# Kernel optimization log

Measured on AMD Instinct MI355X. Metric: run time of the kernel, lower is better.

## Reference

```python
import jax, jax.numpy as jnp
import numpy as np

B, N, C, H, M, CC = 8, 1024, 1280, 20, 77, 768
FF = 4 * C
AQ_BITS = 8
W_BITS = 8


def fq_sym(x, bits=AQ_BITS):
    # per-tensor symmetric fake quant with straight-through estimator
    qmax = 2.0 ** (bits - 1) - 1.0
    delta = jnp.maximum(jnp.max(jnp.abs(x)), 1e-8) / qmax
    q = jnp.clip(jnp.round(x / delta), -qmax - 1.0, qmax) * delta
    return x + jax.lax.stop_gradient(q - x)


def fq_zero(x, bits=W_BITS):
    # asymmetric, always_zero (zero point = 0): for softmax probs in [0,1]
    levels = 2.0 ** bits - 1.0
    delta = jnp.maximum(jnp.max(x), 1e-8) / levels
    q = jnp.clip(jnp.round(x / delta), 0.0, levels) * delta
    return x + jax.lax.stop_gradient(q - x)


def layer_norm(x, g, b, eps=1e-5):
    mu = jnp.mean(x, axis=-1, keepdims=True)
    var = jnp.var(x, axis=-1, keepdims=True)
    return (x - mu) * jax.lax.rsqrt(var + eps) * g + b


def attention(x, ctx, Wq, Wk, Wv, Wo, bo, heads):
    b, n, c = x.shape
    m = ctx.shape[1]
    dh = c // heads
    q = fq_sym(x @ Wq)
    k = fq_sym(ctx @ Wk)
    v = fq_sym(ctx @ Wv)
    q = q.reshape(b, n, heads, dh).transpose(0, 2, 1, 3)
    k = k.reshape(b, m, heads, dh).transpose(0, 2, 1, 3)
    v = v.reshape(b, m, heads, dh).transpose(0, 2, 1, 3)
    scores = jnp.einsum('bhnd,bhmd->bhnm', q, k) * (dh ** -0.5)
    w = jax.nn.softmax(scores, axis=-1)
    w = fq_zero(w)  # quantized softmax weights (forces explicit prob materialization)
    out = jnp.einsum('bhnm,bhmd->bhnd', w, v)
    out = out.transpose(0, 2, 1, 3).reshape(b, n, c)
    return out @ Wo + bo


def geglu_ff(x, W1, b1, W2, b2):
    h = x @ W1 + b1
    a, g = jnp.split(h, 2, axis=-1)
    return (a * jax.nn.gelu(g)) @ W2 + b2


def setup_inputs() -> dict:
    key = jax.random.key(0)
    ks = jax.random.split(key, 16)
    s = 0.02
    return {
        'x': jax.random.normal(ks[0], (B, N, C), jnp.float32),
        'ctx': jax.random.normal(ks[1], (B, M, CC), jnp.float32),
        'ln1_g': jnp.ones((C,), jnp.float32), 'ln1_b': jnp.zeros((C,), jnp.float32),
        'ln2_g': jnp.ones((C,), jnp.float32), 'ln2_b': jnp.zeros((C,), jnp.float32),
        'ln3_g': jnp.ones((C,), jnp.float32), 'ln3_b': jnp.zeros((C,), jnp.float32),
        'Wq1': jax.random.normal(ks[2], (C, C), jnp.float32) * s,
        'Wk1': jax.random.normal(ks[3], (C, C), jnp.float32) * s,
        'Wv1': jax.random.normal(ks[4], (C, C), jnp.float32) * s,
        'Wo1': jax.random.normal(ks[5], (C, C), jnp.float32) * s,
        'bo1': jnp.zeros((C,), jnp.float32),
        'Wq2': jax.random.normal(ks[6], (C, C), jnp.float32) * s,
        'Wk2': jax.random.normal(ks[7], (CC, C), jnp.float32) * s,
        'Wv2': jax.random.normal(ks[8], (CC, C), jnp.float32) * s,
        'Wo2': jax.random.normal(ks[9], (C, C), jnp.float32) * s,
        'bo2': jnp.zeros((C,), jnp.float32),
        'Wff1': jax.random.normal(ks[10], (C, 2 * FF), jnp.float32) * s,
        'bff1': jnp.zeros((2 * FF,), jnp.float32),
        'Wff2': jax.random.normal(ks[11], (FF, C), jnp.float32) * s,
        'bff2': jnp.zeros((C,), jnp.float32),
        'heads': H,
    }


def reference(x, ctx, ln1_g, ln1_b, ln2_g, ln2_b, ln3_g, ln3_b,
              Wq1, Wk1, Wv1, Wo1, bo1, Wq2, Wk2, Wv2, Wo2, bo2,
              Wff1, bff1, Wff2, bff2, heads):
    h = attention(layer_norm(x, ln1_g, ln1_b), layer_norm(x, ln1_g, ln1_b),
                  Wq1, Wk1, Wv1, Wo1, bo1, heads)
    x = x + h
    h = attention(layer_norm(x, ln2_g, ln2_b), ctx, Wq2, Wk2, Wv2, Wo2, bo2, heads)
    x = x + h
    x = x + geglu_ff(layer_norm(x, ln3_g, ln3_b), Wff1, bff1, Wff2, bff2)
    return x
```

## Files before the change

### kernel.cpp

```cpp
#include <hip/hip_runtime.h>

typedef __attribute__((ext_vector_type(8))) short bf16x8;
typedef __attribute__((ext_vector_type(4))) float f32x4;

#define DEV __device__ __forceinline__
#define MF(A, B, CACC) CACC = __builtin_amdgcn_mfma_f32_16x16x32_bf16(A, B, CACC, 0, 0, 0)

DEV ushort f2b(float f) {
  unsigned u = __float_as_uint(f);
  u += 0x7fffu + ((u >> 16) & 1u);
  return (ushort)(u >> 16);
}
DEV float b2f(ushort u) { return __uint_as_float(((unsigned)u) << 16); }

DEV void gl_lds16(ushort* lds_base, const ushort* gp) {
  __builtin_amdgcn_global_load_lds(
      (__attribute__((address_space(1))) const void*)gp,
      (__attribute__((address_space(3))) void*)lds_base, 16, 0, 0);
}

__global__ void k_zero(unsigned* p, int n) {
  int i = blockIdx.x * blockDim.x + threadIdx.x;
  if (i < n) p[i] = 0u;
}
// ... 76 lines not shown
    if (rbase + 0 < M) st1(v0, rbase + 0, c_, ldc, resid, Cf, Cb);
    if (rbase + 1 < M) st1(v1, rbase + 1, c_, ldc, resid, Cf, Cb);
    if (rbase + 2 < M) st1(v2, rbase + 2, c_, ldc, resid, Cf, Cb);
    if (rbase + 3 < M) st1(v3, rbase + 3, c_, ldc, resid, Cf, Cb);
  }
  return am;
}

__global__ __launch_bounds__(256) void k_gemm(
    const ushort* __restrict__ A, int lda,
    const ushort* __restrict__ BT, int ldb,
    float* __restrict__ Cf, ushort* __restrict__ Cb, int ldc,
    const float* __restrict__ bias, const float* __restrict__ resid,
    unsigned* am_slot, int M, int N, int K, int slcN) {
  __shared__ __align__(16) ushort SAB[8192];
  int tid = threadIdx.x;
  int wave = tid >> 6, lane = tid & 63;
  int q = lane >> 4, mi = lane & 15;
  int wr = (wave >> 1) * 64, wc = (wave & 1) * 64;
  int bm0 = blockIdx.y * 128, bn0 = blockIdx.x * 128;
  f32x4 c00 = {}, c01 = {}, c02 = {}, c03 = {};
  f32x4 c10 = {}, c11 = {}, c12 = {}, c13 = {};
  f32x4 c20 = {}, c21 = {}, c22 = {}, c23 = {};
  f32x4 c30 = {}, c31 = {}, c32 = {}, c33 = {};
  for (int k0 = 0; k0 < K; k0 += 32) {
    __syncthreads();
    #pragma unroll
    for (int t = 0; t < 4; t++) {
      int c = wave * 256 + t * 64 + lane;
      const ushort* gp;
      if (c < 512) {
        int r = c >> 2, kc = (c & 3) << 3;
        int gr = bm0 + r; if (gr >= M) gr = M - 1;
        gp = A + (size_t)gr * lda + k0 + kc;
      } else {
        int c2 = c - 512;
        int r = c2 >> 2, kc = (c2 & 3) << 3;
        int gn = bn0 + r; if (gn >= N) gn = N - 1;
        gp = BT + (size_t)gn * ldb + k0 + kc;
      }
      gl_lds16(&SAB[(wave * 256 + t * 64) * 8], gp);
    }
    __syncthreads();
    const ushort* Ab = &SAB[(wr + mi) * 32 + q * 8];
    const ushort* Bb = &SAB[4096 + (wc + mi) * 32 + q * 8];
    bf16x8 a0 = *(const bf16x8*)(Ab);
    bf16x8 a1 = *(const bf16x8*)(Ab + 512);
    bf16x8 a2 = *(const bf16x8*)(Ab + 1024);
    bf16x8 a3 = *(const bf16x8*)(Ab + 1536);
    bf16x8 b0 = *(const bf16x8*)(Bb);
    bf16x8 b1 = *(const bf16x8*)(Bb + 512);
    bf16x8 b2 = *(const bf16x8*)(Bb + 1024);
    bf16x8 b3 = *(const bf16x8*)(Bb + 1536);
    MF(a0, b0, c00); MF(a0, b1, c01); MF(a0, b2, c02); MF(a0, b3, c03);
    MF(a1, b0, c10); MF(a1, b1, c11); MF(a1, b2, c12); MF(a1, b3, c13);
    MF(a2, b0, c20); MF(a2, b1, c21); MF(a2, b2, c22); MF(a2, b3, c23);
    MF(a3, b0, c30); MF(a3, b1, c31); MF(a3, b2, c32); MF(a3, b3, c33);
  }
  int rb = bm0 + wr + q * 4, cb = bn0 + wc + mi;
  float am = 0.f;
  am = fmaxf(am, epi4(c00, rb +  0, cb +  0, M, N, ldc, bias, resid, Cf, Cb));
  am = fmaxf(am, epi4(c01, rb +  0, cb + 16, M, N, ldc, bias, resid, Cf, Cb));
  am = fmaxf(am, epi4(c02, rb +  0, cb + 32, M, N, ldc, bias, resid, Cf, Cb));
  am = fmaxf(am, epi4(c03, rb +  0, cb + 48, M, N, ldc, bias, resid, Cf, Cb));
  am = fmaxf(am, epi4(c10, rb + 16, cb +  0, M, N, ldc, bias, resid, Cf, Cb));
  am = fmaxf(am, epi4(c11, rb + 16, cb + 16, M, N, ldc, bias, resid, Cf, Cb));
  am = fmaxf(am, epi4(c12, rb + 16, cb + 32, M, N, ldc, bias, resid, Cf, Cb));
  am = fmaxf(am, epi4(c13, rb + 16, cb + 48, M, N, ldc, bias, resid, Cf, Cb));
  am = fmaxf(am, epi4(c20, rb + 32, cb +  0, M, N, ldc, bias, resid, Cf, Cb));
  am = fmaxf(am, epi4(c21, rb + 32, cb + 16, M, N, ldc, bias, resid, Cf, Cb));
  am = fmaxf(am, epi4(c22, rb + 32, cb + 32, M, N, ldc, bias, resid, Cf, Cb));
  am = fmaxf(am, epi4(c23, rb + 32, cb + 48, M, N, ldc, bias, resid, Cf, Cb));
  am = fmaxf(am, epi4(c30, rb + 48, cb +  0, M, N, ldc, bias, resid, Cf, Cb));
  am = fmaxf(am, epi4(c31, rb + 48, cb + 16, M, N, ldc, bias, resid, Cf, Cb));
  am = fmaxf(am, epi4(c32, rb + 48, cb + 32, M, N, ldc, bias, resid, Cf, Cb));
  am = fmaxf(am, epi4(c33, rb + 48, cb + 48, M, N, ldc, bias, resid, Cf, Cb));
  if (am_slot) {
    #pragma unroll
    for (int off = 32; off; off >>= 1) am = fmaxf(am, __shfl_down(am, off));
    if (lane == 0) atomicMax(am_slot + bn0 / slcN, __float_as_uint(am));
  }
}

__global__ void k_quant3(const ushort* __restrict__ in, ushort* __restrict__ out,
                         const unsigned* __restrict__ slotb, int n,
                         int colw, int ld, int slcw) {
  int i = blockIdx.x * 256 + threadIdx.x;
  if (i >= n) return;
  int row = i / colw, col = i - row * colw;
  size_t a = (size_t)row * ld + col;
  float delta = fmaxf(__uint_as_float(slotb[col / slcw]), 1e-8f) * (1.f / 127.f);
  float x = b2f(in[a]);
  float y = fminf(fmaxf(rintf(x / delta), -128.f), 127.f) * delta;
  out[a] = f2b(y);
}

__global__ __launch_bounds__(256) void k_vt(const ushort* __restrict__ vq,
    ushort* __restrict__ vT, int H, int Mr, int Mpad, int ldv) {
  __shared__ __align__(16) ushort T[64][72];
  int bh = blockIdx.y, b = bh / H, h = bh % H;
  int m0 = blockIdx.x * 64;
  int tid = threadIdx.x;
  #pragma unroll
  for (int c = tid; c < 512; c += 256) {
    int mm = c >> 3, dc = (c & 7) << 3;
    int m = m0 + mm;
    int4 val = make_int4(0, 0, 0, 0);
    if (m < Mr) val = *(const int4*)(vq + ((size_t)b * Mr + m) * ldv + h * 64 + dc);
    *(int4*)&T[mm][dc] = val;
  }
  __syncthreads();
  #pragma unroll
  for (int c = tid; c < 512; c += 256) {
    int dd = c >> 3, mc = (c & 7) << 3;
    unsigned w0 = (unsigned)T[mc + 0][dd] | ((unsigned)T[mc + 1][dd] << 16);
    unsigned w1 = (unsigned)T[mc + 2][dd] | ((unsigned)T[mc + 3][dd] << 16);
    unsigned w2 = (unsigned)T[mc + 4][dd] | ((unsigned)T[mc + 5][dd] << 16);
    unsigned w3 = (unsigned)T[mc + 6][dd] | ((unsigned)T[mc + 7][dd] << 16);
    int4 val = make_int4((int)w0, (int)w1, (int)w2, (int)w3);
    *(int4*)(vT + ((size_t)bh * 64 + dd) * Mpad + m0 + mc) = val;
  }
}

__global__ __launch_bounds__(256) void k_attn1(
    const ushort* __restrict__ qq, const ushort* __restrict__ kq,
    float2* __restrict__ rs, unsigned* __restrict__ pmax,
    int H, int N, int Mr, int ldq, int ldk, float cs) {
  __shared__ __align__(16) ushort Qs[64][72];
  __shared__ __align__(16) ushort Ks[64][72];
  int tid = threadIdx.x;
  int wave = tid >> 6, lane = tid & 63;
  int q = lane >> 4, mi = lane & 15;
  int bh = blockIdx.y, b = bh / H, h = bh % H;
  int r0 = blockIdx.x * 64;
  #pragma unroll
  for (int c = tid; c < 512; c += 256) {
    int r = c >> 3, dc = (c & 7) << 3;
    *(int4*)&Qs[r][dc] = *(const int4*)(qq + ((size_t)b * N + r0 + r) * ldq + h * 64 + dc);
  }
  float m_run = -3.0e38f, z_run = 0.f;
  int nt = (Mr + 63) >> 6;
  for (int mt = 0; mt < nt; mt++) {
    __syncthreads();
    #pragma unroll
    for (int c = tid; c < 512; c += 256) {
      int mm = c >> 3, dc = (c & 7) << 3;
      int m = mt * 64 + mm;
      int4 val = make_int4(0, 0, 0, 0);
      if (m < Mr) val = *(const int4*)(kq + ((size_t)b * Mr + m) * ldk + h * 64 + dc);
      *(int4*)&Ks[mm][dc] = val;
    }
    __syncthreads();
    f32x4 s0 = {}, s1 = {}, s2 = {}, s3 = {};
    #pragma unroll
    for (int kc = 0; kc < 2; kc++) {
      bf16x8 qv  = *(const bf16x8*)&Qs[wave * 16 + mi][kc * 32 + q * 8];
      bf16x8 k0v = *(const bf16x8*)&Ks[mi][kc * 32 + q * 8];
      bf16x8 k1v = *(const bf16x8*)&Ks[16 + mi][kc * 32 + q * 8];
      bf16x8 k2v = *(const bf16x8*)&Ks[32 + mi][kc * 32 + q * 8];
      bf16x8 k3v = *(const bf16x8*)&Ks[48 + mi][kc * 32 + q * 8];
      MF(k0v, qv, s0); MF(k1v, qv, s1); MF(k2v, qv, s2); MF(k3v, qv, s3);
    }
    int kb = mt * 64 + q * 4;
    float e0  = (kb + 0  < Mr) ? s0.x * cs : -3.0e38f;
    float e1  = (kb + 1  < Mr) ? s0.y * cs : -3.0e38f;
    float e2  = (kb + 2  < Mr) ? s0.z * cs : -3.0e38f;
    float e3  = (kb + 3  < Mr) ? s0.w * cs : -3.0e38f;
    float e4  = (kb + 16 < Mr) ? s1.x * cs : -3.0e38f;
    float e5  = (kb + 17 < Mr) ? s1.y * cs : -3.0e38f;
    float e6  = (kb + 18 < Mr) ? s1.z * cs : -3.0e38f;
    float e7  = (kb + 19 < Mr) ? s1.w * cs : -3.0e38f;
    float e8  = (kb + 32 < Mr) ? s2.x * cs : -3.0e38f;
    float e9  = (kb + 33 < Mr) ? s2.y * cs : -3.0e38f;
    float e10 = (kb + 34 < Mr) ? s2.z * cs : -3.0e38f;
    float e11 = (kb + 35 < Mr) ? s2.w * cs : -3.0e38f;
    float e12 = (kb + 48 < Mr) ? s3.x * cs : -3.0e38f;
    float e13 = (kb + 49 < Mr) ? s3.y * cs : -3.0e38f;
    float e14 = (kb + 50 < Mr) ? s3.z * cs : -3.0e38f;
    float e15 = (kb + 51 < Mr) ? s3.w * cs : -3.0e38f;
    float tm = fmaxf(fmaxf(fmaxf(fmaxf(e0, e1), fmaxf(e2, e3)),
                           fmaxf(fmaxf(e4, e5), fmaxf(e6, e7))),
                     fmaxf(fmaxf(fmaxf(e8, e9), fmaxf(e10, e11)),
                           fmaxf(fmaxf(e12, e13), fmaxf(e14, e15))));
    float mn = fmaxf(m_run, tm);
    float zs = exp2f(e0 - mn)  + exp2f(e1 - mn)  + exp2f(e2 - mn)  + exp2f(e3 - mn)
             + exp2f(e4 - mn)  + exp2f(e5 - mn)  + exp2f(e6 - mn)  + exp2f(e7 - mn)
             + exp2f(e8 - mn)  + exp2f(e9 - mn)  + exp2f(e10 - mn) + exp2f(e11 - mn)
             + exp2f(e12 - mn) + exp2f(e13 - mn) + exp2f(e14 - mn) + exp2f(e15 - mn);
    z_run = z_run * exp2f(m_run - mn) + zs;
    m_run = mn;
  }
  float mo = fmaxf(m_run, __shfl_xor(m_run, 16));
  mo = fmaxf(mo, __shfl_xor(mo, 32));
  float zz = z_run * exp2f(m_run - mo);
  zz += __shfl_xor(zz, 16);
  zz += __shfl_xor(zz, 32);
  if (q == 0) {
    float2 st; st.x = mo; st.y = zz;
    rs[(size_t)bh * N + r0 + wave * 16 + mi] = st;
  }
  float pm = 1.f / zz;
  #pragma unroll
  for (int off = 32; off; off >>= 1) pm = fmaxf(pm, __shfl_down(pm, off));
  if (lane == 0) atomicMax(pmax, __float_as_uint(pm));
}

DEV ushort q8lvl(float s, float cs, float mc) {
  float p = fminf(rintf(exp2f(fmaf(s, cs, -mc))), 255.f);
  return (ushort)(__float_as_uint(p) >> 16);
}

__global__ __launch_bounds__(256) void k_attn2(
    const ushort* __restrict__ qq, const ushort* __restrict__ kq,
    const ushort* __restrict__ vT, const float2* __restrict__ rs,
    const unsigned* __restrict__ pmax, ushort* __restrict__ ao,
    int H, int N, int Mr, int Mpad, int ldq, int ldk, float cs) {
  const int C = 1280;
  __shared__ __align__(16) ushort Qs[64][72];
  __shared__ __align__(16) ushort Ks[64][72];
  __shared__ __align__(16) ushort Vs[64][72];
  __shared__ __align__(16) ushort Ps[64][72];
  int tid = threadIdx.x;
  int wave = tid >> 6, lane = tid & 63;
  int q = lane >> 4, mi = lane & 15;
  int bh = blockIdx.y, b = bh / H, h = bh % H;
  int r0 = blockIdx.x * 64;
  #pragma unroll
  for (int c = tid; c < 512; c += 256) {
    int r = c >> 3, dc = (c & 7) << 3;
    *(int4*)&Qs[r][dc] = *(const int4*)(qq + ((size_t)b * N + r0 + r) * ldq + h * 64 + dc);
  }
  int rbase = wave * 16 + q * 4;
  float delta = fmaxf(__uint_as_float(*pmax), 1e-8f) * (1.f / 255.f);
  float ld = __log2f(delta);
  float2 st0 = rs[(size_t)bh * N + r0 + rbase + 0];
  float2 st1 = rs[(size_t)bh * N + r0 + rbase + 1];
  float2 st2 = rs[(size_t)bh * N + r0 + rbase + 2];
  float2 st3 = rs[(size_t)bh * N + r0 + rbase + 3];
  float mc0 = st0.x + __log2f(st0.y) + ld;
  float mc1 = st1.x + __log2f(st1.y) + ld;
  float mc2 = st2.x + __log2f(st2.y) + ld;
  float mc3 = st3.x + __log2f(st3.y) + ld;
  f32x4 o0 = {}, o1 = {}, o2 = {}, o3 = {};
  int nt = (Mr + 63) >> 6;
  for (int mt = 0; mt < nt; mt++) {
    __syncthreads();
    #pragma unroll
    for (int c = tid; c < 512; c += 256) {
      int mm = c >> 3, dc = (c & 7) << 3;
      int m = mt * 64 + mm;
      int4 val = make_int4(0, 0, 0, 0);
      if (m < Mr) val = *(const int4*)(kq + ((size_t)b * Mr + m) * ldk + h * 64 + dc);
      *(int4*)&Ks[mm][dc] = val;
      *(int4*)&Vs[mm][dc] = *(const int4*)(vT + ((size_t)bh * 64 + mm) * Mpad + mt * 64 + dc);
    }
    __syncthreads();
    f32x4 s0 = {}, s1 = {}, s2 = {}, s3 = {};
    #pragma unroll
    for (int kc = 0; kc < 2; kc++) {
      bf16x8 aq  = *(const bf16x8*)&Qs[wave * 16 + mi][kc * 32 + q * 8];
      bf16x8 k0v = *(const bf16x8*)&Ks[mi][kc * 32 + q * 8];
      bf16x8 k1v = *(const bf16x8*)&Ks[16 + mi][kc * 32 + q * 8];
      bf16x8 k2v = *(const bf16x8*)&Ks[32 + mi][kc * 32 + q * 8];
      bf16x8 k3v = *(const bf16x8*)&Ks[48 + mi][kc * 32 + q * 8];
      MF(aq, k0v, s0); MF(aq, k1v, s1); MF(aq, k2v, s2); MF(aq, k3v, s3);
    }
    int mlim = Mr - mt * 64;
    bool ok0 = (mi      < mlim);
    bool ok1 = (16 + mi < mlim);
    bool ok2 = (32 + mi < mlim);
    bool ok3 = (48 + mi < mlim);
    Ps[rbase + 0][mi]      = ok0 ? q8lvl(s0.x, cs, mc0) : (ushort)0;
    Ps[rbase + 1][mi]      = ok0 ? q8lvl(s0.y, cs, mc1) : (ushort)0;
    Ps[rbase + 2][mi]      = ok0 ? q8lvl(s0.z, cs, mc2) : (ushort)0;
    Ps[rbase + 3][mi]      = ok0 ? q8lvl(s0.w, cs, mc3) : (ushort)0;
    Ps[rbase + 0][16 + mi] = ok1 ? q8lvl(s1.x, cs, mc0) : (ushort)0;
    Ps[rbase + 1][16 + mi] = ok1 ? q8lvl(s1.y, cs, mc1) : (ushort)0;
    Ps[rbase + 2][16 + mi] = ok1 ? q8lvl(s1.z, cs, mc2) : (ushort)0;
    Ps[rbase + 3][16 + mi] = ok1 ? q8lvl(s1.w, cs, mc3) : (ushort)0;
    Ps[rbase + 0][32 + mi] = ok2 ? q8lvl(s2.x, cs, mc0) : (ushort)0;
    Ps[rbase + 1][32 + mi] = ok2 ? q8lvl(s2.y, cs, mc1) : (ushort)0;
    Ps[rbase + 2][32 + mi] = ok2 ? q8lvl(s2.z, cs, mc2) : (ushort)0;
    Ps[rbase + 3][32 + mi] = ok2 ? q8lvl(s2.w, cs, mc3) : (ushort)0;
    Ps[rbase + 0][48 + mi] = ok3 ? q8lvl(s3.x, cs, mc0) : (ushort)0;
    Ps[rbase + 1][48 + mi] = ok3 ? q8lvl(s3.y, cs, mc1) : (ushort)0;
    Ps[rbase + 2][48 + mi] = ok3 ? q8lvl(s3.z, cs, mc2) : (ushort)0;
    Ps[rbase + 3][48 + mi] = ok3 ? q8lvl(s3.w, cs, mc3) : (ushort)0;
    asm volatile("s_waitcnt lgkmcnt(0)" ::: "memory");
    __builtin_amdgcn_sched_barrier(0);
    #pragma unroll
    for (int kc = 0; kc < 2; kc++) {
      bf16x8 ap = *(const bf16x8*)&Ps[wave * 16 + mi][kc * 32 + q * 8];
      bf16x8 v0 = *(const bf16x8*)&Vs[mi][kc * 32 + q * 8];
      bf16x8 v1 = *(const bf16x8*)&Vs[16 + mi][kc * 32 + q * 8];
      bf16x8 v2 = *(const bf16x8*)&Vs[32 + mi][kc * 32 + q * 8];
      bf16x8 v3 = *(const bf16x8*)&Vs[48 + mi][kc * 32 + q * 8];
      MF(ap, v0, o0); MF(ap, v1, o1); MF(ap, v2, o2); MF(ap, v3, o3);
    }
  }
  int rr = r0 + wave * 16 + q * 4;
  size_t base = ((size_t)b * N + rr) * C + h * 64 + mi;
  ao[base]              = f2b(o0.x * delta); ao[base + C]          = f2b(o0.y * delta);
  ao[base + 2 * C]      = f2b(o0.z * delta); ao[base + 3 * C]      = f2b(o0.w * delta);
  ao[base + 16]         = f2b(o1.x * delta); ao[base + C + 16]     = f2b(o1.y * delta);
  ao[base + 2 * C + 16] = f2b(o1.z * delta); ao[base + 3 * C + 16] = f2b(o1.w * delta);
  ao[base + 32]         = f2b(o2.x * delta); ao[base + C + 32]     = f2b(o2.y * delta);
  ao[base + 2 * C + 32] = f2b(o2.z * delta); ao[base + 3 * C + 32] = f2b(o2.w * delta);
  ao[base + 48]         = f2b(o3.x * delta); ao[base + C + 48]     = f2b(o3.y * delta);
  ao[base + 2 * C + 48] = f2b(o3.z * delta); ao[base + 3 * C + 48] = f2b(o3.w * delta);
}

#define BAR __builtin_amdgcn_s_barrier()
#define LGKM0 do { asm volatile("s_waitcnt lgkmcnt(0)" ::: "memory"); \
                   __builtin_amdgcn_sched_barrier(0); } while (0)
#define VM6 asm volatile("s_waitcnt vmcnt(6)" ::: "memory")
#define VM0 asm volatile("s_waitcnt vmcnt(0)" ::: "memory")
#define PRIO1 __builtin_amdgcn_s_setprio(1)
#define PRIO0 __builtin_amdgcn_s_setprio(0)

#define RDA01(P) do { \
  fa00 = *(const bf16x8*)&(P)[c0];        fa01 = *(const bf16x8*)&(P)[c1]; \
  fa10 = *(const bf16x8*)&(P)[1024 + c0]; fa11 = *(const bf16x8*)&(P)[1024 + c1]; } while (0)
#define RDA23(P) do { \
  fa20 = *(const bf16x8*)&(P)[2048 + c0]; fa21 = *(const bf16x8*)&(P)[2048 + c1]; \
  fa30 = *(const bf16x8*)&(P)[3072 + c0]; fa31 = *(const bf16x8*)&(P)[3072 + c1]; } while (0)
#define RDB(P, H) do { \
  b00 = *(const bf16x8*)&(P)[(H) + c0];        b01 = *(const bf16x8*)&(P)[(H) + c1]; \
  b10 = *(const bf16x8*)&(P)[(H) + 1024 + c0]; b11 = *(const bf16x8*)&(P)[(H) + 1024 + c1]; \
  b20 = *(const bf16x8*)&(P)[(H) + 2048 + c0]; b21 = *(const bf16x8*)&(P)[(H) + 2048 + c1]; \
  b30 = *(const bf16x8*)&(P)[(H) + 3072 + c0]; b31 = *(const bf16x8*)&(P)[(H) + 3072 + c1]; } while (0)
#define RDB8(P) RDB(P, 0)

#define MM8(AX0, AX1, AY0, AY1, C0, C1, C2, C3, D0, D1, D2, D3) \
  MF(AX0, b00, C0); MF(AX1, b01, C0); MF(AX0, b10, C1); MF(AX1, b11, C1); \
  MF(AX0, b20, C2); MF(AX1, b21, C2); MF(AX0, b30, C3); MF(AX1, b31, C3); \
  MF(AY0, b00, D0); MF(AY1, b01, D0); MF(AY0, b10, D1); MF(AY1, b11, D1); \
  MF(AY0, b20, D2); MF(AY1, b21, D2); MF(AY0, b30, D3); MF(AY1, b31, D3)

#define GB8(AP, BP, DB, KT) \
  RDA01(AP); RDB8(BP); \
  stB(DB, KT, 0); stB(DB, KT, 1); stA(DB, KT, 0); \
  BAR; LGKM0; \
  PRIO1; MM8(fa00, fa01, fa10, fa11, c00, c01, c02, c03, c10, c11, c12, c13); PRIO0; \
  BAR; \
  RDA23(AP); \
  stA(DB, KT, 1); stA(DB, KT, 2); stA(DB, KT, 3); \
  BAR; LGKM0; \
  PRIO1; MM8(fa20, fa21, fa30, fa31, c20, c21, c22, c23, c30, c31, c32, c33); PRIO0; \
  VM6; BAR;

#define GT8(AP, BP) \
  RDA01(AP); RDB8(BP); \
  BAR; LGKM0; \
  PRIO1; MM8(fa00, fa01, fa10, fa11, c00, c01, c02, c03, c10, c11, c12, c13); PRIO0; \
  BAR; \
  RDA23(AP); \
  BAR; LGKM0; \
  PRIO1; MM8(fa20, fa21, fa30, fa31, c20, c21, c22, c23, c30, c31, c32, c33); PRIO0;

__global__ __launch_bounds__(512) void k_gemm8(
    const ushort* __restrict__ A, int lda,
    const ushort* __restrict__ BT, int ldb,
    float* __restrict__ Cf, ushort* __restrict__ Cb, int ldc,
    const float* __restrict__ bias, const float* __restrict__ resid,
    unsigned* am_slot, int M, int N, int K, int slcN) {
  __shared__ __align__(16) ushort SAB[73728];
  int tid = threadIdx.x;
  int wave = tid >> 6, lane = tid & 63;
  int q = lane >> 4, mi = lane & 15;
  int wm = wave >> 1, wn = wave & 1;
  int lr = lane >> 3;
  int lc = ((lane & 7) ^ lr) * 8;

  int NBN = N >> 7;
  int nblk = (M >> 8) * NBN;
  int cpx = nblk >> 3;
  int wg = blockIdx.x;
  int swz = (wg & 7) * cpx + (wg >> 3);
  int bm0 = (swz / NBN) << 8, bn0 = (swz % NBN) << 7;

  const int swzr = (mi & 7) * 8;
  int c0 = (q * 8) ^ swzr, c1 = (32 + q * 8) ^ swzr;
  const ushort* A0p = &SAB[(wm * 64 + mi) * 64];
  const ushort* B0p = &SAB[16384 + (wn * 64 + mi) * 64];
  const ushort* A1p = A0p + 24576; const ushort* B1p = B0p + 24576;
  const ushort* A2p = A0p + 49152; const ushort* B2p = B0p + 49152;

  const ushort* gA = A  + (size_t)(bm0 + wave * 8 + lr) * lda + lc;
  const ushort* gB = BT + (size_t)(bn0 + wave * 8 + lr) * ldb + lc;
  ushort* lA = &SAB[wave * 512];
  ushort* lB = &SAB[16384 + wave * 512];

// ... 193 lines not shown
  EPIN(0, cA00, cG00, cA10, cG10, cA20, cG20, cA30, cG30);
  EPIN(1, cA01, cG01, cA11, cG11, cA21, cG21, cA31, cG31);
  EPIN(2, cA02, cG02, cA12, cG12, cA22, cG22, cA32, cG32);
  EPIN(3, cA03, cG03, cA13, cG13, cA23, cG23, cA33, cG33);
}

extern "C" void kernel_launch(void* const* d_in, const int* in_sizes, int n_in,
                              void* d_out, int out_size, void* d_ws, size_t ws_size,
                              hipStream_t stream) {
  const float* x_in = (const float*)d_in[0];
  const float* ctx  = (const float*)d_in[1];
  const float* ln1g = (const float*)d_in[2];
  const float* ln1b = (const float*)d_in[3];
  const float* ln2g = (const float*)d_in[4];
  const float* ln2b = (const float*)d_in[5];
  const float* ln3g = (const float*)d_in[6];
  const float* ln3b = (const float*)d_in[7];
  const float* Wq1  = (const float*)d_in[8];
  const float* Wk1  = (const float*)d_in[9];
  const float* Wv1  = (const float*)d_in[10];
  const float* Wo1  = (const float*)d_in[11];
  const float* bo1  = (const float*)d_in[12];
  const float* Wq2  = (const float*)d_in[13];
  const float* Wk2  = (const float*)d_in[14];
  const float* Wv2  = (const float*)d_in[15];
  const float* Wo2  = (const float*)d_in[16];
  const float* bo2  = (const float*)d_in[17];
  const float* Wff1 = (const float*)d_in[18];
  const float* bff1 = (const float*)d_in[19];
  const float* Wff2 = (const float*)d_in[20];
  const float* bff2 = (const float*)d_in[21];
  float* out = (float*)d_out;

  const int NR = 8192;
  const int C = 1280, H = 20, Nseq = 1024, CC = 768;
  const int MR2 = 616;
  const float CS = 0.18033688011112042f;

  char* ws = (char*)d_ws;
  size_t off = 0;
  auto alloc = [&](size_t bytes) -> void* {
    void* p = ws + off;
    off += (bytes + 255) & ~(size_t)255;
    return p;
  };
  unsigned* scal = (unsigned*)alloc(64);
  ushort* Wq1T  = (ushort*)alloc((size_t)C * C * 2);
  ushort* Wk1T  = (ushort*)alloc((size_t)C * C * 2);
  ushort* Wv1T  = (ushort*)alloc((size_t)C * C * 2);
  ushort* Wo1T  = (ushort*)alloc((size_t)C * C * 2);
  ushort* Wq2T  = (ushort*)alloc((size_t)C * C * 2);
  ushort* Wk2T  = (ushort*)alloc((size_t)C * CC * 2);
  ushort* Wv2T  = (ushort*)alloc((size_t)C * CC * 2);
  ushort* Wo2T  = (ushort*)alloc((size_t)C * C * 2);
  ushort* WF1T  = (ushort*)alloc((size_t)10240 * C * 2);
  ushort* WF2T  = (ushort*)alloc((size_t)C * 5120 * 2);
  ushort* LN    = (ushort*)alloc((size_t)NR * C * 2);
  size_t regionR = off;
  ushort* QKV   = (ushort*)alloc((size_t)NR * 3840 * 2);
  ushort* VT    = (ushort*)alloc((size_t)160 * 64 * 1024 * 2);
  float2* RS    = (float2*)alloc((size_t)160 * 1024 * 8);
  ushort* CTXB  = (ushort*)alloc((size_t)MR2 * CC * 2);
  ushort* KV2   = (ushort*)alloc((size_t)MR2 * 2560 * 2);
  size_t need = off;
  ushort* AO = LN;
  ushort* GG = (ushort*)(ws + regionR);
  if (ws_size < need) return;

  k_zero<<<1, 64, 0, stream>>>(scal, 8);
  k_wt<<<dim3(40, 40), 256, 0, stream>>>(Wq1, Wq1T, C, C);
  k_wt<<<dim3(40, 40), 256, 0, stream>>>(Wk1, Wk1T, C, C);
  k_wt<<<dim3(40, 40), 256, 0, stream>>>(Wv1, Wv1T, C, C);
  k_wt<<<dim3(40, 40), 256, 0, stream>>>(Wo1, Wo1T, C, C);
  k_wt<<<dim3(40, 40), 256, 0, stream>>>(Wq2, Wq2T, C, C);
  k_wt<<<dim3(40, 24), 256, 0, stream>>>(Wk2, Wk2T, CC, C);
  k_wt<<<dim3(40, 24), 256, 0, stream>>>(Wv2, Wv2T, CC, C);
  k_wt<<<dim3(40, 40), 256, 0, stream>>>(Wo2, Wo2T, C, C);
  k_wt<<<dim3(320, 40), 256, 0, stream>>>(Wff1, WF1T, C, 10240);
  k_wt<<<dim3(40, 160), 256, 0, stream>>>(Wff2, WF2T, 5120, C);

  k_ln<<<NR, 256, 0, stream>>>(x_in, ln1g, ln1b, LN);
  k_gemm8<<<dim3(960), 512, 0, stream>>>(LN, C, Wq1T, C, nullptr, QKV, 3840,
                                         nullptr, nullptr, scal + 0, NR, 3840, C, 1280);
  k_quant3<<<(NR * 3840 + 255) / 256, 256, 0, stream>>>(QKV, QKV, scal + 0,
                                                        NR * 3840, 3840, 3840, 1280);
  k_vt<<<dim3(16, 160), 256, 0, stream>>>(QKV + 2560, VT, H, 1024, 1024, 3840);
  k_attn1<<<dim3(16, 160), 256, 0, stream>>>(QKV, QKV + 1280, RS, scal + 3,
                                             H, Nseq, 1024, 3840, 3840, CS);
  k_attn2<<<dim3(16, 160), 256, 0, stream>>>(QKV, QKV + 1280, VT, RS, scal + 3, AO,
                                             H, Nseq, 1024, 1024, 3840, 3840, CS);
  k_gemm8<<<dim3(320), 512, 0, stream>>>(AO, C, Wo1T, C, out, nullptr, C,
                                         bo1, x_in, nullptr, NR, C, C, C);

  k_ln<<<NR, 256, 0, stream>>>(out, ln2g, ln2b, LN);
  k_gemm8<<<dim3(320), 512, 0, stream>>>(LN, C, Wq2T, C, nullptr, QKV, 3840,
                                         nullptr, nullptr, scal + 4, NR, C, C, C);
  k_quant3<<<(NR * C + 255) / 256, 256, 0, stream>>>(QKV, QKV, scal + 4,
                                                     NR * C, 1280, 3840, 1280);
  k_cvt<<<(MR2 * CC + 255) / 256, 256, 0, stream>>>(ctx, CTXB, MR2 * CC);
  k_gemm<<<dim3(20, 5), 256, 0, stream>>>(CTXB, CC, Wk2T, CC, nullptr, KV2, 2560,
                                          nullptr, nullptr, scal + 5, MR2, 2560, CC, 1280);
  k_quant3<<<(MR2 * 2560 + 255) / 256, 256, 0, stream>>>(KV2, KV2, scal + 5,
                                                         MR2 * 2560, 2560, 2560, 1280);
  k_vt<<<dim3(2, 160), 256, 0, stream>>>(KV2 + 1280, VT, H, 77, 128, 2560);
  k_attn1<<<dim3(16, 160), 256, 0, stream>>>(QKV, KV2, RS, scal + 7,
                                             H, Nseq, 77, 3840, 2560, CS);
  k_attn2<<<dim3(16, 160), 256, 0, stream>>>(QKV, KV2, VT, RS, scal + 7, AO,
                                             H, Nseq, 77, 128, 3840, 2560, CS);
  k_gemm8<<<dim3(320), 512, 0, stream>>>(AO, C, Wo2T, C, out, nullptr, C,
                                         bo2, out, nullptr, NR, C, C, C);

  k_ln<<<NR, 256, 0, stream>>>(out, ln3g, ln3b, LN);
  k_ff1_8p<<<dim3(1280), 512, 0, stream>>>(LN, WF1T, bff1, GG);
  k_gemm8<<<dim3(320), 512, 0, stream>>>(GG, 5120, WF2T, 5120, out, nullptr, C,
                                         bff2, out, nullptr, NR, C, 5120, C);
}
```

Measured before the change: 1.686 ms.

## Double query rows per attention block and vectorize quantization kernel

New measurement: 1.551 ms. 8.0% less time.

```diff
diff --git a/kernel.cpp b/kernel.cpp
--- a/kernel.cpp
+++ b/kernel.cpp
@@ -182,17 +182,24 @@
   }
 }
 
-__global__ void k_quant3(const ushort* __restrict__ in, ushort* __restrict__ out,
-                         const unsigned* __restrict__ slotb, int n,
-                         int colw, int ld, int slcw) {
+__global__ void k_quant8(const ushort* __restrict__ in, ushort* __restrict__ out,
+                         const unsigned* __restrict__ slotb, int n8,
+                         int colw8, int ld, int slcw) {
   int i = blockIdx.x * 256 + threadIdx.x;
-  if (i >= n) return;
-  int row = i / colw, col = i - row * colw;
+  if (i >= n8) return;
+  int row = i / colw8, c8 = i - row * colw8;
+  int col = c8 * 8;
   size_t a = (size_t)row * ld + col;
   float delta = fmaxf(__uint_as_float(slotb[col / slcw]), 1e-8f) * (1.f / 127.f);
-  float x = b2f(in[a]);
-  float y = fminf(fmaxf(rintf(x / delta), -128.f), 127.f) * delta;
-  out[a] = f2b(y);
+  bf16x8 v = *(const bf16x8*)(in + a);
+  bf16x8 r;
+  #pragma unroll
+  for (int j = 0; j < 8; j++) {
+    float x = b2f((ushort)v[j]);
+    float y = fminf(fmaxf(rintf(x / delta), -128.f), 127.f) * delta;
+    r[j] = (short)f2b(y);
+  }
+  *(bf16x8*)(out + a) = r;
 }
 
 __global__ __launch_bounds__(256) void k_vt(const ushort* __restrict__ vq,
@@ -222,23 +229,53 @@
   }
 }
 
+#define NEGI -3.0e38f
+#define ONLUPD(SA, SB, SC, SD, MRUN, ZRUN) do { \
+  float e0  = b0_  ? (SA).x * cs : NEGI; \
+  float e1  = b1_  ? (SA).y * cs : NEGI; \
+  float e2  = b2_  ? (SA).z * cs : NEGI; \
+  float e3  = b3_  ? (SA).w * cs : NEGI; \
+  float e4  = b4_  ? (SB).x * cs : NEGI; \
+  float e5  = b5_  ? (SB).y * cs : NEGI; \
+  float e6  = b6_  ? (SB).z * cs : NEGI; \
+  float e7  = b7_  ? (SB).w * cs : NEGI; \
+  float e8  = b8_  ? (SC).x * cs : NEGI; \
+  float e9  = b9_  ? (SC).y * cs : NEGI; \
+  float e10 = b10_ ? (SC).z * cs : NEGI; \
+  float e11 = b11_ ? (SC).w * cs : NEGI; \
+  float e12 = b12_ ? (SD).x * cs : NEGI; \
+  float e13 = b13_ ? (SD).y * cs : NEGI; \
+  float e14 = b14_ ? (SD).z * cs : NEGI; \
+  float e15 = b15_ ? (SD).w * cs : NEGI; \
+  float tm = fmaxf(fmaxf(fmaxf(fmaxf(e0, e1), fmaxf(e2, e3)), \
+                         fmaxf(fmaxf(e4, e5), fmaxf(e6, e7))), \
+                   fmaxf(fmaxf(fmaxf(e8, e9), fmaxf(e10, e11)), \
+                         fmaxf(fmaxf(e12, e13), fmaxf(e14, e15)))); \
+  float mn = fmaxf(MRUN, tm); \
+  float zs = exp2f(e0 - mn)  + exp2f(e1 - mn)  + exp2f(e2 - mn)  + exp2f(e3 - mn) \
+           + exp2f(e4 - mn)  + exp2f(e5 - mn)  + exp2f(e6 - mn)  + exp2f(e7 - mn) \
+           + exp2f(e8 - mn)  + exp2f(e9 - mn)  + exp2f(e10 - mn) + exp2f(e11 - mn) \
+           + exp2f(e12 - mn) + exp2f(e13 - mn) + exp2f(e14 - mn) + exp2f(e15 - mn); \
+  ZRUN = ZRUN * exp2f(MRUN - mn) + zs; MRUN = mn; \
+} while (0)
+
 __global__ __launch_bounds__(256) void k_attn1(
     const ushort* __restrict__ qq, const ushort* __restrict__ kq,
     float2* __restrict__ rs, unsigned* __restrict__ pmax,
     int H, int N, int Mr, int ldq, int ldk, float cs) {
-  __shared__ __align__(16) ushort Qs[64][72];
+  __shared__ __align__(16) ushort Qs[128][72];
   __shared__ __align__(16) ushort Ks[64][72];
   int tid = threadIdx.x;
   int wave = tid >> 6, lane = tid & 63;
   int q = lane >> 4, mi = lane & 15;
   int bh = blockIdx.y, b = bh / H, h = bh % H;
-  int r0 = blockIdx.x * 64;
+  int r0 = blockIdx.x * 128;
   #pragma unroll
-  for (int c = tid; c < 512; c += 256) {
+  for (int c = tid; c < 1024; c += 256) {
     int r = c >> 3, dc = (c & 7) << 3;
     *(int4*)&Qs[r][dc] = *(const int4*)(qq + ((size_t)b * N + r0 + r) * ldq + h * 64 + dc);
   }
-  float m_run = -3.0e38f, z_run = 0.f;
+  float m0r = NEGI, z0r = 0.f, m1r = NEGI, z1r = 0.f;
   int nt = (Mr + 63) >> 6;
   for (int mt = 0; mt < nt; mt++) {
     __syncthreads();
@@ -252,54 +289,43 @@
     }
     __syncthreads();
     f32x4 s0 = {}, s1 = {}, s2 = {}, s3 = {};
+    f32x4 s4 = {}, s5 = {}, s6 = {}, s7 = {};
     #pragma unroll
     for (int kc = 0; kc < 2; kc++) {
-      bf16x8 qv  = *(const bf16x8*)&Qs[wave * 16 + mi][kc * 32 + q * 8];
+      bf16x8 qv0 = *(const bf16x8*)&Qs[wave * 32 + mi][kc * 32 + q * 8];
+      bf16x8 qv1 = *(const bf16x8*)&Qs[wave * 32 + 16 + mi][kc * 32 + q * 8];
       bf16x8 k0v = *(const bf16x8*)&Ks[mi][kc * 32 + q * 8];
       bf16x8 k1v = *(const bf16x8*)&Ks[16 + mi][kc * 32 + q * 8];
       bf16x8 k2v = *(const bf16x8*)&Ks[32 + mi][kc * 32 + q * 8];
       bf16x8 k3v = *(const bf16x8*)&Ks[48 + mi][kc * 32 + q * 8];
-      MF(k0v, qv, s0); MF(k1v, qv, s1); MF(k2v, qv, s2); MF(k3v, qv, s3);
+      MF(k0v, qv0, s0); MF(k1v, qv0, s1); MF(k2v, qv0, s2); MF(k3v, qv0, s3);
+      MF(k0v, qv1, s4); MF(k1v, qv1, s5); MF(k2v, qv1, s6); MF(k3v, qv1, s7);
     }
     int kb = mt * 64 + q * 4;
-    float e0  = (kb + 0  < Mr) ? s0.x * cs : -3.0e38f;
-    float e1  = (kb + 1  < Mr) ? s0.y * cs : -3.0e38f;
-    float e2  = (kb + 2  < Mr) ? s0.z * cs : -3.0e38f;
-    float e3  = (kb + 3  < Mr) ? s0.w * cs : -3.0e38f;
-    float e4  = (kb + 16 < Mr) ? s1.x * cs : -3.0e38f;
-    float e5  = (kb + 17 < Mr) ? s1.y * cs : -3.0e38f;
-    float e6  = (kb + 18 < Mr) ? s1.z * cs : -3.0e38f;
-    float e7  = (kb + 19 < Mr) ? s1.w * cs : -3.0e38f;
-    float e8  = (kb + 32 < Mr) ? s2.x * cs : -3.0e38f;
-    float e9  = (kb + 33 < Mr) ? s2.y * cs : -3.0e38f;
-    float e10 = (kb + 34 < Mr) ? s2.z * cs : -3.0e38f;
-    float e11 = (kb + 35 < Mr) ? s2.w * cs : -3.0e38f;
-    float e12 = (kb + 48 < Mr) ? s3.x * cs : -3.0e38f;
-    float e13 = (kb + 49 < Mr) ? s3.y * cs : -3.0e38f;
-    float e14 = (kb + 50 < Mr) ? s3.z * cs : -3.0e38f;
-    float e15 = (kb + 51 < Mr) ? s3.w * cs : -3.0e38f;
-    float tm = fmaxf(fmaxf(fmaxf(fmaxf(e0, e1), fmaxf(e2, e3)),
-                           fmaxf(fmaxf(e4, e5), fmaxf(e6, e7))),
-                     fmaxf(fmaxf(fmaxf(e8, e9), fmaxf(e10, e11)),
-                           fmaxf(fmaxf(e12, e13), fmaxf(e14, e15))));
-    float mn = fmaxf(m_run, tm);
-    float zs = exp2f(e0 - mn)  + exp2f(e1 - mn)  + exp2f(e2 - mn)  + exp2f(e3 - mn)
-             + exp2f(e4 - mn)  + exp2f(e5 - mn)  + exp2f(e6 - mn)  + exp2f(e7 - mn)
-             + exp2f(e8 - mn)  + exp2f(e9 - mn)  + exp2f(e10 - mn) + exp2f(e11 - mn)
-             + exp2f(e12 - mn) + exp2f(e13 - mn) + exp2f(e14 - mn) + exp2f(e15 - mn);
-    z_run = z_run * exp2f(m_run - mn) + zs;
-    m_run = mn;
-  }
-  float mo = fmaxf(m_run, __shfl_xor(m_run, 16));
-  mo = fmaxf(mo, __shfl_xor(mo, 32));
-  float zz = z_run * exp2f(m_run - mo);
-  zz += __shfl_xor(zz, 16);
-  zz += __shfl_xor(zz, 32);
+    bool b0_  = kb + 0  < Mr, b1_  = kb + 1  < Mr, b2_  = kb + 2  < Mr, b3_  = kb + 3  < Mr;
+    bool b4_  = kb + 16 < Mr, b5_  = kb + 17 < Mr, b6_  = kb + 18 < Mr, b7_  = kb + 19 < Mr;
+    bool b8_  = kb + 32 < Mr, b9_  = kb + 33 < Mr, b10_ = kb + 34 < Mr, b11_ = kb + 35 < Mr;
+    bool b12_ = kb + 48 < Mr, b13_ = kb + 49 < Mr, b14_ = kb + 50 < Mr, b15_ = kb + 51 < Mr;
+    ONLUPD(s0, s1, s2, s3, m0r, z0r);
+    ONLUPD(s4, s5, s6, s7, m1r, z1r);
+  }
+  float mo0 = fmaxf(m0r, __shfl_xor(m0r, 16));
+  mo0 = fmaxf(mo0, __shfl_xor(mo0, 32));
+  float zz0 = z0r * exp2f(m0r - mo0);
+  zz0 += __shfl_xor(zz0, 16);
+  zz0 += __shfl_xor(zz0, 32);
+  float mo1 = fmaxf(m1r, __shfl_xor(m1r, 16));
+  mo1 = fmaxf(mo1, __shfl_xor(mo1, 32));
+  float zz1 = z1r * exp2f(m1r - mo1);
+  zz1 += __shfl_xor(zz1, 16);
+  zz1 += __shfl_xor(zz1, 32);
   if (q == 0) {
-    float2 st; st.x = mo; st.y = zz;
-    rs[(size_t)bh * N + r0 + wave * 16 + mi] = st;
-  }
-  float pm = 1.f / zz;
+    float2 st; st.x = mo0; st.y = zz0;
+    rs[(size_t)bh * N + r0 + wave * 32 + mi] = st;
+    st.x = mo1; st.y = zz1;
+    rs[(size_t)bh * N + r0 + wave * 32 + 16 + mi] = st;
+  }
+  float pm = fmaxf(1.f / zz0, 1.f / zz1);
   #pragma unroll
   for (int off = 32; off; off >>= 1) pm = fmaxf(pm, __shfl_down(pm, off));
   if (lane == 0) atomicMax(pmax, __float_as_uint(pm));
@@ -309,6 +335,37 @@
   float p = fminf(rintf(exp2f(fmaf(s, cs, -mc))), 255.f);
   return (ushort)(__float_as_uint(p) >> 16);
 }
+
+#define PWR(RB, SA, SB, SC, SD, M0_, M1_, M2_, M3_) do { \
+  Ps[(RB) + 0][mi]      = ok0 ? q8lvl((SA).x, cs, M0_) : (ushort)0; \
+  Ps[(RB) + 1][mi]      = ok0 ? q8lvl((SA).y, cs, M1_) : (ushort)0; \
+  Ps[(RB) + 2][mi]      = ok0 ? q8lvl((SA).z, cs, M2_) : (ushort)0; \
+  Ps[(RB) + 3][mi]      = ok0 ? q8lvl((SA).w, cs, M3_) : (ushort)0; \
+  Ps[(RB) + 0][16 + mi] = ok1 ? q8lvl((SB).x, cs, M0_) : (ushort)0; \
+  Ps[(RB) + 1][16 + mi] = ok1 ? q8lvl((SB).y, cs, M1_) : (ushort)0; \
+  Ps[(RB) + 2][16 + mi] = ok1 ? q8lvl((SB).z, cs, M2_) : (ushort)0; \
+  Ps[(RB) + 3][16 + mi] = ok1 ? q8lvl((SB).w, cs, M3_) : (ushort)0; \
+  Ps[(RB) + 0][32 + mi] = ok2 ? q8lvl((SC).x, cs, M0_) : (ushort)0; \
+  Ps[(RB) + 1][32 + mi] = ok2 ? q8lvl((SC).y, cs, M1_) : (ushort)0; \
+  Ps[(RB) + 2][32 + mi] = ok2 ? q8lvl((SC).z, cs, M2_) : (ushort)0; \
+  Ps[(RB) + 3][32 + mi] = ok2 ? q8lvl((SC).w, cs, M3_) : (ushort)0; \
+  Ps[(RB) + 0][48 + mi] = ok3 ? q8lvl((SD).x, cs, M0_) : (ushort)0; \
+  Ps[(RB) + 1][48 + mi] = ok3 ? q8lvl((SD).y, cs, M1_) : (ushort)0; \
+  Ps[(RB) + 2][48 + mi] = ok3 ? q8lvl((SD).z, cs, M2_) : (ushort)0; \
+  Ps[(RB) + 3][48 + mi] = ok3 ? q8lvl((SD).w, cs, M3_) : (ushort)0; \
+} while (0)
+
+#define OSTORE(RRBASE, OA, OB, OC, OD) do { \
+  size_t base = ((size_t)b * N + (RRBASE)) * C + h * 64 + mi; \
+  ao[base]              = f2b((OA).x * delta); ao[base + C]          = f2b((OA).y * delta); \
+  ao[base + 2 * C]      = f2b((OA).z * delta); ao[base + 3 * C]      = f2b((OA).w * delta); \
+  ao[base + 16]         = f2b((OB).x * delta); ao[base + C + 16]     = f2b((OB).y * delta); \
+  ao[base + 2 * C + 16] = f2b((OB).z * delta); ao[base + 3 * C + 16] = f2b((OB).w * delta); \
+  ao[base + 32]         = f2b((OC).x * delta); ao[base + C + 32]     = f2b((OC).y * delta); \
+  ao[base + 2 * C + 32] = f2b((OC).z * delta); ao[base + 3 * C + 32] = f2b((OC).w * delta); \
+  ao[base + 48]         = f2b((OD).x * delta); ao[base + C + 48]     = f2b((OD).y * delta); \
+  ao[base + 2 * C + 48] = f2b((OD).z * delta); ao[base + 3 * C + 48] = f2b((OD).w * delta); \
+} while (0)
 
 __global__ __launch_bounds__(256) void k_attn2(
     const ushort* __restrict__ qq, const ushort* __restrict__ kq,
@@ -316,32 +373,41 @@
     const unsigned* __restrict__ pmax, ushort* __restrict__ ao,
     int H, int N, int Mr, int Mpad, int ldq, int ldk, float cs) {
   const int C = 1280;
-  __shared__ __align__(16) ushort Qs[64][72];
+  __shared__ __align__(16) ushort Qs[128][72];
   __shared__ __align__(16) ushort Ks[64][72];
   __shared__ __align__(16) ushort Vs[64][72];
-  __shared__ __align__(16) ushort Ps[64][72];
+  __shared__ __align__(16) ushort Ps[128][72];
   int tid = threadIdx.x;
   int wave = tid >> 6, lane = tid & 63;
   int q = lane >> 4, mi = lane & 15;
   int bh = blockIdx.y, b = bh / H, h = bh % H;
-  int r0 = blockIdx.x * 64;
+  int r0 = blockIdx.x * 128;
   #pragma unroll
-  for (int c = tid; c < 512; c += 256) {
+  for (int c = tid; c < 1024; c += 256) {
     int r = c >> 3, dc = (c & 7) << 3;
     *(int4*)&Qs[r][dc] = *(const int4*)(qq + ((size_t)b * N + r0 + r) * ldq + h * 64 + dc);
   }
-  int rbase = wave * 16 + q * 4;
+  int rb0 = wave * 32 + q * 4, rb1 = rb0 + 16;
   float delta = fmaxf(__uint_as_float(*pmax), 1e-8f) * (1.f / 255.f);
-  float ld = __log2f(delta);
-  float2 st0 = rs[(size_t)bh * N + r0 + rbase + 0];
-  float2 st1 = rs[(size_t)bh * N + r0 + rbase + 1];
-  float2 st2 = rs[(size_t)bh * N + r0 + rbase + 2];
-  float2 st3 = rs[(size_t)bh * N + r0 + rbase + 3];
-  float mc0 = st0.x + __log2f(st0.y) + ld;
-  float mc1 = st1.x + __log2f(st1.y) + ld;
-  float mc2 = st2.x + __log2f(st2.y) + ld;
-  float mc3 = st3.x + __log2f(st3.y) + ld;
+  float ldl = __log2f(delta);
+  float2 u0 = rs[(size_t)bh * N + r0 + rb0 + 0];
+  float2 u1 = rs[(size_t)bh * N + r0 + rb0 + 1];
+  float2 u2 = rs[(size_t)bh * N + r0 + rb0 + 2];
+  float2 u3 = rs[(size_t)bh * N + r0 + rb0 + 3];
+  float2 u4 = rs[(size_t)bh * N + r0 + rb1 + 0];
+  float2 u5 = rs[(size_t)bh * N + r0 + rb1 + 1];
+  float2 u6 = rs[(size_t)bh * N + r0 + rb1 + 2];
+  float2 u7 = rs[(size_t)bh * N + r0 + rb1 + 3];
+  float mc0 = u0.x + __log2f(u0.y) + ldl;
+  float mc1 = u1.x + __log2f(u1.y) + ldl;
+  float mc2 = u2.x + __log2f(u2.y) + ldl;
+  float mc3 = u3.x + __log2f(u3.y) + ldl;
+  float mc4 = u4.x + __log2f(u4.y) + ldl;
+  float mc5 = u5.x + __log2f(u5.y) + ldl;
+  float mc6 = u6.x + __log2f(u6.y) + ldl;
+  float mc7 = u7.x + __log2f(u7.y) + ldl;
   f32x4 o0 = {}, o1 = {}, o2 = {}, o3 = {};
+  f32x4 o4 = {}, o5 = {}, o6 = {}, o7 = {};
   int nt = (Mr + 63) >> 6;
   for (int mt = 0; mt < nt; mt++) {
     __syncthreads();
@@ -356,58 +422,42 @@
     }
     __syncthreads();
     f32x4 s0 = {}, s1 = {}, s2 = {}, s3 = {};
+    f32x4 s4 = {}, s5 = {}, s6 = {}, s7 = {};
     #pragma unroll
     for (int kc = 0; kc < 2; kc++) {
-      bf16x8 aq  = *(const bf16x8*)&Qs[wave * 16 + mi][kc * 32 + q * 8];
+      bf16x8 aq0 = *(const bf16x8*)&Qs[wave * 32 + mi][kc * 32 + q * 8];
+      bf16x8 aq1 = *(const bf16x8*)&Qs[wave * 32 + 16 + mi][kc * 32 + q * 8];
       bf16x8 k0v = *(const bf16x8*)&Ks[mi][kc * 32 + q * 8];
       bf16x8 k1v = *(const bf16x8*)&Ks[16 + mi][kc * 32 + q * 8];
       bf16x8 k2v = *(const bf16x8*)&Ks[32 + mi][kc * 32 + q * 8];
       bf16x8 k3v = *(const bf16x8*)&Ks[48 + mi][kc * 32 + q * 8];
-      MF(aq, k0v, s0); MF(aq, k1v, s1); MF(aq, k2v, s2); MF(aq, k3v, s3);
+      MF(aq0, k0v, s0); MF(aq0, k1v, s1); MF(aq0, k2v, s2); MF(aq0, k3v, s3);
+      MF(aq1, k0v, s4); MF(aq1, k1v, s5); MF(aq1, k2v, s6); MF(aq1, k3v, s7);
     }
     int mlim = Mr - mt * 64;
     bool ok0 = (mi      < mlim);
     bool ok1 = (16 + mi < mlim);
     bool ok2 = (32 + mi < mlim);
     bool ok3 = (48 + mi < mlim);
-    Ps[rbase + 0][mi]      = ok0 ? q8lvl(s0.x, cs, mc0) : (ushort)0;
-    Ps[rbase + 1][mi]      = ok0 ? q8lvl(s0.y, cs, mc1) : (ushort)0;
-    Ps[rbase + 2][mi]      = ok0 ? q8lvl(s0.z, cs, mc2) : (ushort)0;
-    Ps[rbase + 3][mi]      = ok0 ? q8lvl(s0.w, cs, mc3) : (ushort)0;
-    Ps[rbase + 0][16 + mi] = ok1 ? q8lvl(s1.x, cs, mc0) : (ushort)0;
-    Ps[rbase + 1][16 + mi] = ok1 ? q8lvl(s1.y, cs, mc1) : (ushort)0;
-    Ps[rbase + 2][16 + mi] = ok1 ? q8lvl(s1.z, cs, mc2) : (ushort)0;
-    Ps[rbase + 3][16 + mi] = ok1 ? q8lvl(s1.w, cs, mc3) : (ushort)0;
-    Ps[rbase + 0][32 + mi] = ok2 ? q8lvl(s2.x, cs, mc0) : (ushort)0;
-    Ps[rbase + 1][32 + mi] = ok2 ? q8lvl(s2.y, cs, mc1) : (ushort)0;
-    Ps[rbase + 2][32 + mi] = ok2 ? q8lvl(s2.z, cs, mc2) : (ushort)0;
-    Ps[rbase + 3][32 + mi] = ok2 ? q8lvl(s2.w, cs, mc3) : (ushort)0;
-    Ps[rbase + 0][48 + mi] = ok3 ? q8lvl(s3.x, cs, mc0) : (ushort)0;
-    Ps[rbase + 1][48 + mi] = ok3 ? q8lvl(s3.y, cs, mc1) : (ushort)0;
-    Ps[rbase + 2][48 + mi] = ok3 ? q8lvl(s3.z, cs, mc2) : (ushort)0;
-    Ps[rbase + 3][48 + mi] = ok3 ? q8lvl(s3.w, cs, mc3) : (ushort)0;
+    PWR(rb0, s0, s1, s2, s3, mc0, mc1, mc2, mc3);
+    PWR(rb1, s4, s5, s6, s7, mc4, mc5, mc6, mc7);
     asm volatile("s_waitcnt lgkmcnt(0)" ::: "memory");
     __builtin_amdgcn_sched_barrier(0);
     #pragma unroll
     for (int kc = 0; kc < 2; kc++) {
-      bf16x8 ap = *(const bf16x8*)&Ps[wave * 16 + mi][kc * 32 + q * 8];
+      bf16x8 ap0 = *(const bf16x8*)&Ps[wave * 32 + mi][kc * 32 + q * 8];
+      bf16x8 ap1 = *(const bf16x8*)&Ps[wave * 32 + 16 + mi][kc * 32 + q * 8];
       bf16x8 v0 = *(const bf16x8*)&Vs[mi][kc * 32 + q * 8];
       bf16x8 v1 = *(const bf16x8*)&Vs[16 + mi][kc * 32 + q * 8];
       bf16x8 v2 = *(const bf16x8*)&Vs[32 + mi][kc * 32 + q * 8];
       bf16x8 v3 = *(const bf16x8*)&Vs[48 + mi][kc * 32 + q * 8];
-      MF(ap, v0, o0); MF(ap, v1, o1); MF(ap, v2, o2); MF(ap, v3, o3);
+      MF(ap0, v0, o0); MF(ap0, v1, o1); MF(ap0, v2, o2); MF(ap0, v3, o3);
+      MF(ap1, v0, o4); MF(ap1, v1, o5); MF(ap1, v2, o6); MF(ap1, v3, o7);
     }
   }
-  int rr = r0 + wave * 16 + q * 4;
-  size_t base = ((size_t)b * N + rr) * C + h * 64 + mi;
-  ao[base]              = f2b(o0.x * delta); ao[base + C]          = f2b(o0.y * delta);
-  ao[base + 2 * C]      = f2b(o0.z * delta); ao[base + 3 * C]      = f2b(o0.w * delta);
-  ao[base + 16]         = f2b(o1.x * delta); ao[base + C + 16]     = f2b(o1.y * delta);
-  ao[base + 2 * C + 16] = f2b(o1.z * delta); ao[base + 3 * C + 16] = f2b(o1.w * delta);
-  ao[base + 32]         = f2b(o2.x * delta); ao[base + C + 32]     = f2b(o2.y * delta);
-  ao[base + 2 * C + 32] = f2b(o2.z * delta); ao[base + 3 * C + 32] = f2b(o2.w * delta);
-  ao[base + 48]         = f2b(o3.x * delta); ao[base + C + 48]     = f2b(o3.y * delta);
-  ao[base + 2 * C + 48] = f2b(o3.z * delta); ao[base + 3 * C + 48] = f2b(o3.w * delta);
+  int rr0 = r0 + wave * 32 + q * 4;
+  OSTORE(rr0, o0, o1, o2, o3);
+  OSTORE(rr0 + 16, o4, o5, o6, o7);
 }
 
 #define BAR __builtin_amdgcn_s_barrier()
@@ -767,31 +817,31 @@
   k_ln<<<NR, 256, 0, stream>>>(x_in, ln1g, ln1b, LN);
   k_gemm8<<<dim3(960), 512, 0, stream>>>(LN, C, Wq1T, C, nullptr, QKV, 3840,
                                          nullptr, nullptr, scal + 0, NR, 3840, C, 1280);
-  k_quant3<<<(NR * 3840 + 255) / 256, 256, 0, stream>>>(QKV, QKV, scal + 0,
-                                                        NR * 3840, 3840, 3840, 1280);
+  k_quant8<<<(NR * 3840 / 8 + 255) / 256, 256, 0, stream>>>(QKV, QKV, scal + 0,
+                                                            NR * 480, 480, 3840, 1280);
   k_vt<<<dim3(16, 160), 256, 0, stream>>>(QKV + 2560, VT, H, 1024, 1024, 3840);
-  k_attn1<<<dim3(16, 160), 256, 0, stream>>>(QKV, QKV + 1280, RS, scal + 3,
-                                             H, Nseq, 1024, 3840, 3840, CS);
-  k_attn2<<<dim3(16, 160), 256, 0, stream>>>(QKV, QKV + 1280, VT, RS, scal + 3, AO,
-                                             H, Nseq, 1024, 1024, 3840, 3840, CS);
+  k_attn1<<<dim3(8, 160), 256, 0, stream>>>(QKV, QKV + 1280, RS, scal + 3,
+                                            H, Nseq, 1024, 3840, 3840, CS);
+  k_attn2<<<dim3(8, 160), 256, 0, stream>>>(QKV, QKV + 1280, VT, RS, scal + 3, AO,
+                                            H, Nseq, 1024, 1024, 3840, 3840, CS);
   k_gemm8<<<dim3(320), 512, 0, stream>>>(AO, C, Wo1T, C, out, nullptr, C,
                                          bo1, x_in, nullptr, NR, C, C, C);
 
   k_ln<<<NR, 256, 0, stream>>>(out, ln2g, ln2b, LN);
   k_gemm8<<<dim3(320), 512, 0, stream>>>(LN, C, Wq2T, C, nullptr, QKV, 3840,
                                          nullptr, nullptr, scal + 4, NR, C, C, C);
-  k_quant3<<<(NR * C + 255) / 256, 256, 0, stream>>>(QKV, QKV, scal + 4,
-                                                     NR * C, 1280, 3840, 1280);
+  k_quant8<<<(NR * C / 8 + 255) / 256, 256, 0, stream>>>(QKV, QKV, scal + 4,
+                                                         NR * 160, 160, 3840, 1280);
   k_cvt<<<(MR2 * CC + 255) / 256, 256, 0, stream>>>(ctx, CTXB, MR2 * CC);
   k_gemm<<<dim3(20, 5), 256, 0, stream>>>(CTXB, CC, Wk2T, CC, nullptr, KV2, 2560,
                                           nullptr, nullptr, scal + 5, MR2, 2560, CC, 1280);
-  k_quant3<<<(MR2 * 2560 + 255) / 256, 256, 0, stream>>>(KV2, KV2, scal + 5,
-                                                         MR2 * 2560, 2560, 2560, 1280);
+  k_quant8<<<(MR2 * 2560 / 8 + 255) / 256, 256, 0, stream>>>(KV2, KV2, scal + 5,
+                                                             MR2 * 320, 320, 2560, 1280);
   k_vt<<<dim3(2, 160), 256, 0, stream>>>(KV2 + 1280, VT, H, 77, 128, 2560);
-  k_attn1<<<dim3(16, 160), 256, 0, stream>>>(QKV, KV2, RS, scal + 7,
-                                             H, Nseq, 77, 3840, 2560, CS);
-  k_attn2<<<dim3(16, 160), 256, 0, stream>>>(QKV, KV2, VT, RS, scal + 7, AO,
-                                             H, Nseq, 77, 128, 3840, 2560, CS);
+  k_attn1<<<dim3(8, 160), 256, 0, stream>>>(QKV, KV2, RS, scal + 7,
+                                            H, Nseq, 77, 3840, 2560, CS);
+  k_attn2<<<dim3(8, 160), 256, 0, stream>>>(QKV, KV2, VT, RS, scal + 7, AO,
+                                            H, Nseq, 77, 128, 3840, 2560, CS);
   k_gemm8<<<dim3(320), 512, 0, stream>>>(AO, C, Wo2T, C, out, nullptr, C,
                                          bo2, out, nullptr, NR, C, C, C);
 
```
